# Optimization experiments

Measured on AMD Instinct MI355X. Metric: run time of the kernel, lower is better.

Reference implementation:

```python
import jax, jax.numpy as jnp
import numpy as np

TEMPERATURE = 8.0  # sqrt(d_k=64)
MASK_FILL = -1e10


def setup_inputs() -> dict:
    key = jax.random.key(0)
    kq, kk, kv, km = jax.random.split(key, 4)
    b, lq, lk, dk, dv = 32, 2048, 2048, 64, 64
    q = jax.random.normal(kq, (b, lq, dk), dtype=jnp.float32)
    k = jax.random.normal(kk, (b, lk, dk), dtype=jnp.float32)
    v = jax.random.normal(kv, (b, lk, dv), dtype=jnp.float32)
    mask = jax.random.randint(km, (b, lq, lk), 0, 2).astype(jnp.bool_)
    return {"q": q, "k": k, "v": v, "mask": mask}


def reference(q, k, v, mask):
    # attn = q @ k^T / temperature, masked_fill, softmax over keys (dim=2)
    attn = jnp.einsum("bqd,bkd->bqk", q, k) / TEMPERATURE
    attn = jnp.where(mask, MASK_FILL, attn)
    attn = jax.nn.softmax(attn, axis=2)
    # dropout p=0.0 (eval/deterministic reference) -> identity
    output = jnp.einsum("bqk,bkv->bqv", attn, v)
    return (output, attn)
```

## Files before the change

### kernel.cpp

```cpp
#include <hip/hip_runtime.h>
#include <cstdint>
#include <cstddef>

#define B_   32
#define LQ   2048
#define LK   2048
#define DK   64
#define DV   64
#define TQ   16
#define LDP  2056

typedef short bf16x8 __attribute__((ext_vector_type(8)));
typedef float f32x4  __attribute__((ext_vector_type(4)));
typedef int   i32x4  __attribute__((ext_vector_type(4)));

#define KSCALE 0.1803368801111204f

__device__ __forceinline__ short f2bf(float f) {
  unsigned u = __builtin_bit_cast(unsigned, f);
  u += 0x7fffu + ((u >> 16) & 1u);
  return (short)(u >> 16);
}
__device__ __forceinline__ float bflo(unsigned u) { return __builtin_bit_cast(float, u << 16); }
__device__ __forceinline__ float bfhi(unsigned u) { return __builtin_bit_cast(float, u & 0xffff0000u); }

__device__ __forceinline__ bf16x8 pack8(float4 a, float4 b) {
  bf16x8 r;
  r[0]=f2bf(a.x); r[1]=f2bf(a.y); r[2]=f2bf(a.z); r[3]=f2bf(a.w);
  r[4]=f2bf(b.x); r[5]=f2bf(b.y); r[6]=f2bf(b.z); r[7]=f2bf(b.w);
  return r;
}

__global__ __launch_bounds__(512, 4) void sdpa_kernel(
    const float* __restrict__ q, const float* __restrict__ k,
    const float* __restrict__ v, const int* __restrict__ mask,
    float* __restrict__ out, float* __restrict__ attn) {
  __shared__ short P[TQ][LDP];
  __shared__ float rowsum[TQ];
  __shared__ float rinv[TQ];

  const int tid  = threadIdx.x;
  const int wave = tid >> 6;
  const int lane = tid & 63;
  const int quad = lane >> 4;
  const int l15  = lane & 15;
  const int b     = blockIdx.y;
  const int qbase = blockIdx.x * TQ;

  const float* qr = q + ((size_t)b * LQ + qbase + l15) * DK + quad * 8;
  bf16x8 qa0 = pack8(*(const float4*)(qr),      *(const float4*)(qr + 4));
  bf16x8 qa1 = pack8(*(const float4*)(qr + 32), *(const float4*)(qr + 36));

  const float* kbase = k + (size_t)b * LK * DK + (size_t)l15 * DK + quad * 8;
  const f32x4 z4 = {0.f, 0.f, 0.f, 0.f};

  float4 kp0, kp1, kp2, kp3;
  int nt = wave;
  {
    const float* kr = kbase + (size_t)nt * (16 * DK);
    kp0 = *(const float4*)(kr);      kp1 = *(const float4*)(kr + 4);
    kp2 = *(const float4*)(kr + 32); kp3 = *(const float4*)(kr + 36);
  }
  #pragma unroll 1
  for (int i = 0; i < 16; ++i) {
    float4 kc0 = kp0, kc1 = kp1, kc2 = kp2, kc3 = kp3;
    const int ntc = nt;
    nt += 8;
    if (i != 15) {
      const float* kr = kbase + (size_t)nt * (16 * DK);
      kp0 = *(const float4*)(kr);      kp1 = *(const float4*)(kr + 4);
      kp2 = *(const float4*)(kr + 32); kp3 = *(const float4*)(kr + 36);
    }
    bf16x8 kb0 = pack8(kc0, kc1);
    bf16x8 kb1 = pack8(kc2, kc3);
    f32x4 acc0 = __builtin_amdgcn_mfma_f32_16x16x32_bf16(qa0, kb0, z4, 0, 0, 0);
    acc0       = __builtin_amdgcn_mfma_f32_16x16x32_bf16(qa1, kb1, acc0, 0, 0, 0);
    const int col = ntc * 16 + l15;
    #pragma unroll
    for (int r = 0; r < 4; ++r) {
      P[quad * 4 + r][col] = f2bf(__builtin_amdgcn_exp2f(acc0[r] * KSCALE));
    }
  }
  __syncthreads();

  #pragma unroll
  for (int j = 0; j < 2; ++j) {
    const int row = wave * 2 + j;
    const int* mrow = mask + ((size_t)b * LQ + qbase + row) * LK + lane * 4;
    i32x4 mv[8];
    #pragma unroll
    for (int c = 0; c < 8; ++c)
      mv[c] = __builtin_nontemporal_load((const i32x4*)(mrow + c * 256));
    float rs = 0.0f;
    #pragma unroll
    for (int c = 0; c < 8; ++c) {
      uint2 u = *(const uint2*)&P[row][c * 256 + lane * 4];
      unsigned x0 = mv[c][0] ? 0u : (u.x & 0x0000ffffu);
      unsigned x1 = mv[c][1] ? 0u : (u.x & 0xffff0000u);
      unsigned y0 = mv[c][2] ? 0u : (u.y & 0x0000ffffu);
      unsigned y1 = mv[c][3] ? 0u : (u.y & 0xffff0000u);
      u.x = x0 | x1;
      u.y = y0 | y1;
      *(uint2*)&P[row][c * 256 + lane * 4] = u;
      rs += bflo(u.x) + bfhi(u.x) + bflo(u.y) + bfhi(u.y);
    }
    #pragma unroll
    for (int off = 1; off < 64; off <<= 1) rs += __shfl_xor(rs, off);
    if (lane == 0) rowsum[row] = rs;
  }
  __syncthreads();
  if (tid < TQ) rinv[tid] = 1.0f / rowsum[tid];
  __syncthreads();

  if (wave < 4) {
    const float* vbase = v + (size_t)b * LK * DV + wave * 16 + l15;
    f32x4 o0 = z4;
    float fva[8], fvb[8];
    #pragma unroll
    for (int j = 0; j < 8; ++j) {
      fva[j] = vbase[(size_t)(quad * 8 + j) * DV];
      fvb[j] = vbase[(size_t)(32 + quad * 8 + j) * DV];
    }
    #pragma unroll 1
    for (int kt = 0; kt < 64; kt += 2) {
      float fc[8];
      #pragma unroll
      for (int j = 0; j < 8; ++j) fc[j] = fva[j];
      if (kt != 62) {
        #pragma unroll
        for (int j = 0; j < 8; ++j)
          fva[j] = vbase[(size_t)((kt + 2) * 32 + quad * 8 + j) * DV];
      }
      bf16x8 bv0;
      #pragma unroll
      for (int j = 0; j < 8; ++j) bv0[j] = f2bf(fc[j]);
      bf16x8 a0 = *(const bf16x8*)&P[l15][kt * 32 + quad * 8];
      o0 = __builtin_amdgcn_mfma_f32_16x16x32_bf16(a0, bv0, o0, 0, 0, 0);

      #pragma unroll
      for (int j = 0; j < 8; ++j) fc[j] = fvb[j];
      if (kt != 62) {
        #pragma unroll
        for (int j = 0; j < 8; ++j)
          fvb[j] = vbase[(size_t)((kt + 3) * 32 + quad * 8 + j) * DV];
      }
      bf16x8 bv1;
      #pragma unroll
      for (int j = 0; j < 8; ++j) bv1[j] = f2bf(fc[j]);
      bf16x8 a1 = *(const bf16x8*)&P[l15][(kt + 1) * 32 + quad * 8];
      o0 = __builtin_amdgcn_mfma_f32_16x16x32_bf16(a1, bv1, o0, 0, 0, 0);
    }
    #pragma unroll
    for (int r = 0; r < 4; ++r) {
      const int row0 = quad * 4 + r;
      out[((size_t)b * LQ + qbase + row0) * DV + wave * 16 + l15] = o0[r] * rinv[row0];
    }
  } else {
    const int ww = wave - 4;
    float* abase = attn + ((size_t)b * LQ + qbase) * (size_t)LK;
    #pragma unroll 1
    for (int j = 0; j < 4; ++j) {
      const int row = ww * 4 + j;
      const float ri = rinv[row];
      float* dst = abase + (size_t)row * LK;
      #pragma unroll
      for (int it = 0; it < 8; ++it) {
        const int c = it * 256 + lane * 4;
        uint2 u = *(const uint2*)&P[row][c];
        f32x4 val;
        val[0] = bflo(u.x) * ri;
        val[1] = bfhi(u.x) * ri;
        val[2] = bflo(u.y) * ri;
        val[3] = bfhi(u.y) * ri;
        __builtin_nontemporal_store(val, (f32x4*)(dst + c));
      }
    }
  }
}

extern "C" void kernel_launch(void* const* d_in, const int* in_sizes, int n_in,
                              void* d_out, int out_size, void* d_ws, size_t ws_size,
                              hipStream_t stream) {
  (void)in_sizes; (void)n_in; (void)out_size; (void)d_ws; (void)ws_size;
  const float* q    = (const float*)d_in[0];
  const float* k    = (const float*)d_in[1];
  const float* v    = (const float*)d_in[2];
  const int*   mask = (const int*)d_in[3];
  float* out  = (float*)d_out;
  float* attn = out + (size_t)B_ * LQ * DV;
  dim3 grid(LQ / TQ, B_);
  sdpa_kernel<<<grid, 512, 0, stream>>>(q, k, v, mask, out, attn);
}
```

Baseline: 1.268 ms.

## Fuse mask into QK pass and stage unnormalized fp32 attn in global memory

Mask values are now loaded, software-prefetched, inside the QK^T/exp loop, and masked probabilities are zeroed there. This removes the separate shared-memory masking pass and its extra barrier. Row sums are built per lane and combined with shuffles plus shared-memory atomics. Unnormalized fp32 probabilities are written straight to the attn output, then reread, scaled by the reciprocal row sum and rewritten. This keeps attn at full precision but adds a global read-modify-write of the large attn tensor, which relies on cache hits, and uses narrower scalar mask loads.

Result: slower. 1.425 ms (+12.3%).

```diff
diff --git a/kernel.cpp b/kernel.cpp
--- a/kernel.cpp
+++ b/kernel.cpp
@@ -12,7 +12,6 @@
 
 typedef short bf16x8 __attribute__((ext_vector_type(8)));
 typedef float f32x4  __attribute__((ext_vector_type(4)));
-typedef int   i32x4  __attribute__((ext_vector_type(4)));
 
 #define KSCALE 0.1803368801111204f
 
@@ -21,8 +20,6 @@
   u += 0x7fffu + ((u >> 16) & 1u);
   return (short)(u >> 16);
 }
-__device__ __forceinline__ float bflo(unsigned u) { return __builtin_bit_cast(float, u << 16); }
-__device__ __forceinline__ float bfhi(unsigned u) { return __builtin_bit_cast(float, u & 0xffff0000u); }
 
 __device__ __forceinline__ bf16x8 pack8(float4 a, float4 b) {
   bf16x8 r;
@@ -47,66 +44,71 @@
   const int b     = blockIdx.y;
   const int qbase = blockIdx.x * TQ;
 
+  if (tid < TQ) rowsum[tid] = 0.0f;
+  __syncthreads();
+
   const float* qr = q + ((size_t)b * LQ + qbase + l15) * DK + quad * 8;
   bf16x8 qa0 = pack8(*(const float4*)(qr),      *(const float4*)(qr + 4));
   bf16x8 qa1 = pack8(*(const float4*)(qr + 32), *(const float4*)(qr + 36));
 
   const float* kbase = k + (size_t)b * LK * DK + (size_t)l15 * DK + quad * 8;
+  const int*   mbase = mask + ((size_t)b * LQ + qbase + quad * 4) * (size_t)LK + l15;
+  float*       abase = attn + ((size_t)b * LQ + qbase + quad * 4) * (size_t)LK + l15;
   const f32x4 z4 = {0.f, 0.f, 0.f, 0.f};
 
   float4 kp0, kp1, kp2, kp3;
-  int nt = wave;
+  int mp0[4], mp1[4];
   {
-    const float* kr = kbase + (size_t)nt * (16 * DK);
+    const float* kr = kbase + (size_t)wave * (16 * DK);
     kp0 = *(const float4*)(kr);      kp1 = *(const float4*)(kr + 4);
     kp2 = *(const float4*)(kr + 32); kp3 = *(const float4*)(kr + 36);
+    const int* mr0 = mbase + wave * 16;
+    const int* mr1 = mbase + (wave + 8) * 16;
+    #pragma unroll
+    for (int r = 0; r < 4; ++r) {
+      mp0[r] = __builtin_nontemporal_load(mr0 + (size_t)r * LK);
+      mp1[r] = __builtin_nontemporal_load(mr1 + (size_t)r * LK);
+    }
   }
+  float sum0[4] = {0,0,0,0};
   #pragma unroll 1
-  for (int i = 0; i < 16; ++i) {
+  for (int j = 0; j < 16; ++j) {
     float4 kc0 = kp0, kc1 = kp1, kc2 = kp2, kc3 = kp3;
-    const int ntc = nt;
-    nt += 8;
-    if (i != 15) {
-      const float* kr = kbase + (size_t)nt * (16 * DK);
+    int mc[4];
+    #pragma unroll
+    for (int r = 0; r < 4; ++r) { mc[r] = mp0[r]; mp0[r] = mp1[r]; }
+    const int ntc = wave + 8 * j;
+    if (j < 15) {
+      const float* kr = kbase + (size_t)(ntc + 8) * (16 * DK);
       kp0 = *(const float4*)(kr);      kp1 = *(const float4*)(kr + 4);
       kp2 = *(const float4*)(kr + 32); kp3 = *(const float4*)(kr + 36);
+    }
+    if (j < 14) {
+      const int* mr = mbase + (ntc + 16) * 16;
+      #pragma unroll
+      for (int r = 0; r < 4; ++r)
+        mp1[r] = __builtin_nontemporal_load(mr + (size_t)r * LK);
     }
     bf16x8 kb0 = pack8(kc0, kc1);
     bf16x8 kb1 = pack8(kc2, kc3);
     f32x4 acc0 = __builtin_amdgcn_mfma_f32_16x16x32_bf16(qa0, kb0, z4, 0, 0, 0);
     acc0       = __builtin_amdgcn_mfma_f32_16x16x32_bf16(qa1, kb1, acc0, 0, 0, 0);
     const int col = ntc * 16 + l15;
+    float* ast = abase + ntc * 16;
     #pragma unroll
     for (int r = 0; r < 4; ++r) {
-      P[quad * 4 + r][col] = f2bf(__builtin_amdgcn_exp2f(acc0[r] * KSCALE));
+      float p = mc[r] ? 0.0f : __builtin_amdgcn_exp2f(acc0[r] * KSCALE);
+      P[quad * 4 + r][col] = f2bf(p);
+      ast[(size_t)r * LK] = p;
+      sum0[r] += p;
     }
   }
-  __syncthreads();
-
   #pragma unroll
-  for (int j = 0; j < 2; ++j) {
-    const int row = wave * 2 + j;
-    const int* mrow = mask + ((size_t)b * LQ + qbase + row) * LK + lane * 4;
-    i32x4 mv[8];
+  for (int r = 0; r < 4; ++r) {
+    float s0 = sum0[r];
     #pragma unroll
-    for (int c = 0; c < 8; ++c)
-      mv[c] = __builtin_nontemporal_load((const i32x4*)(mrow + c * 256));
-    float rs = 0.0f;
-    #pragma unroll
-    for (int c = 0; c < 8; ++c) {
-      uint2 u = *(const uint2*)&P[row][c * 256 + lane * 4];
-      unsigned x0 = mv[c][0] ? 0u : (u.x & 0x0000ffffu);
-      unsigned x1 = mv[c][1] ? 0u : (u.x & 0xffff0000u);
-      unsigned y0 = mv[c][2] ? 0u : (u.y & 0x0000ffffu);
-      unsigned y1 = mv[c][3] ? 0u : (u.y & 0xffff0000u);
-      u.x = x0 | x1;
-      u.y = y0 | y1;
-      *(uint2*)&P[row][c * 256 + lane * 4] = u;
-      rs += bflo(u.x) + bfhi(u.x) + bflo(u.y) + bfhi(u.y);
-    }
-    #pragma unroll
-    for (int off = 1; off < 64; off <<= 1) rs += __shfl_xor(rs, off);
-    if (lane == 0) rowsum[row] = rs;
+    for (int off = 1; off < 16; off <<= 1) s0 += __shfl_xor(s0, off);
+    if (l15 == 0) atomicAdd(&rowsum[quad * 4 + r], s0);
   }
   __syncthreads();
   if (tid < TQ) rinv[tid] = 1.0f / rowsum[tid];
@@ -157,22 +159,21 @@
     }
   } else {
     const int ww = wave - 4;
-    float* abase = attn + ((size_t)b * LQ + qbase) * (size_t)LK;
+    float* arow = attn + ((size_t)b * LQ + qbase) * (size_t)LK + lane * 4;
     #pragma unroll 1
     for (int j = 0; j < 4; ++j) {
       const int row = ww * 4 + j;
       const float ri = rinv[row];
-      float* dst = abase + (size_t)row * LK;
+      float* dst = arow + (size_t)row * LK;
+      f32x4 vals[8];
+      #pragma unroll
+      for (int it = 0; it < 8; ++it)
+        vals[it] = *(const f32x4*)(dst + it * 256);
       #pragma unroll
       for (int it = 0; it < 8; ++it) {
-        const int c = it * 256 + lane * 4;
-        uint2 u = *(const uint2*)&P[row][c];
-        f32x4 val;
-        val[0] = bflo(u.x) * ri;
-        val[1] = bfhi(u.x) * ri;
-        val[2] = bflo(u.y) * ri;
-        val[3] = bfhi(u.y) * ri;
-        __builtin_nontemporal_store(val, (f32x4*)(dst + c));
+        f32x4 vv = vals[it];
+        vv[0] *= ri; vv[1] *= ri; vv[2] *= ri; vv[3] *= ri;
+        *(f32x4*)(dst + it * 256) = vv;
       }
     }
   }
```
